# Kernel optimization log

Hardware: AMD Instinct MI355X
Metric: run time of the kernel (lower is better)

## Reference

```python
import jax, jax.numpy as jnp
import numpy as np

EPS = 1e-6


def _build_cayley():
    # Blade ordering of the CEGNN CliffordAlgebra for Cl(3,0): combinations order
    # 1, e1, e2, e3, e12, e13, e23, e123. Metric (1,1,1) => e_k^2 = +1.
    blades = [(), (0,), (1,), (2,), (0, 1), (0, 2), (1, 2), (0, 1, 2)]
    index = {b: i for i, b in enumerate(blades)}
    cayley = np.zeros((8, 8, 8), dtype=np.float32)
    for i, a in enumerate(blades):
        for j, b in enumerate(blades):
            arr = list(a) + list(b)
            sign = 1
            # bubble sort, counting transpositions of anticommuting generators
            for p in range(len(arr)):
                for q in range(len(arr) - 1):
                    if arr[q] > arr[q + 1]:
                        arr[q], arr[q + 1] = arr[q + 1], arr[q]
                        sign = -sign
            # contract equal adjacent generators (e_k e_k = +1)
            out = []
            q = 0
            while q < len(arr):
                if q + 1 < len(arr) and arr[q] == arr[q + 1]:
                    q += 2
                else:
                    out.append(arr[q])
                    q += 1
            cayley[i, j, index[tuple(out)]] = sign
    return cayley


_CAYLEY = jnp.asarray(_build_cayley())  # (8, 8, 8)


def _mvlinear(x, W, b):
    # MVLinear(subspaces=False): channel mixing shared across blades,
    # bias embedded into the scalar (grade-0) blade only.
    y = jnp.einsum("bmi,nm->bni", x, W)
    return y.at[:, :, 0].add(b)


def setup_inputs() -> dict:
    key = jax.random.key(0)
    ks = jax.random.split(key, 7)
    B, Cin, Ch, Cout = 16384, 512, 512, 512
    s = 1.0 / np.sqrt(Cin)
    return {
        "vec1": jax.random.normal(ks[0], (B, Cin, 8), dtype=jnp.float32),
        "W_left": jax.random.normal(ks[1], (Ch, Cin), dtype=jnp.float32) * s,
        "b_left": jax.random.normal(ks[2], (Ch,), dtype=jnp.float32) * 0.01,
        "W_right": jax.random.normal(ks[3], (Ch, Cin), dtype=jnp.float32) * s,
        "b_right": jax.random.normal(ks[4], (Ch,), dtype=jnp.float32) * 0.01,
        "W_out": jax.random.normal(ks[5], (Cout, Ch), dtype=jnp.float32) * s,
        "b_out": jax.random.normal(ks[6], (Cout,), dtype=jnp.float32) * 0.01,
        "a_norm": jnp.ones((Cout,), dtype=jnp.float32),
    }


def reference(vec1, W_left, b_left, W_right, b_right, W_out, b_out, a_norm):
    vec_right = _mvlinear(vec1, W_right, b_right)   # (B, Ch, 8)
    vec_left = _mvlinear(vec1, W_left, b_left)      # (B, Ch, 8)
    # geometric product via the sparse Cayley table of Cl(3,0)
    gp = jnp.einsum("bmi,ijk,bmj->bmk", vec_left, _CAYLEY, vec_right)
    out = _mvlinear(gp, W_out, b_out)               # (B, Cout, 8)
    # MVLayerNorm: per-multivector quadratic-form norm (all-positive metric =>
    # sqrt of sum of squared blade coefficients), averaged over channels.
    norm = jnp.sqrt(jnp.sum(out * out, axis=-1, keepdims=True))  # (B, Cout, 1)
    norm = jnp.mean(norm, axis=1, keepdims=True) + EPS           # (B, 1, 1)
    return a_norm[None, :, None] * out / norm
```

## Files before the change

kernel.cpp:

```cpp
#include <hip/hip_runtime.h>
#include <cstdint>
#include <cstddef>

typedef _Float16 f16;
typedef __attribute__((ext_vector_type(8))) _Float16 f16x8;
typedef __attribute__((ext_vector_type(4))) _Float16 f16x4;
typedef __attribute__((ext_vector_type(4))) float f32x4;

#define MFMA_F16(a, b, c) __builtin_amdgcn_mfma_f32_16x16x32_f16((a), (b), (c), 0, 0, 0)

#define GL2LDS(gsrc, ldst)                                                  \
    __builtin_amdgcn_global_load_lds(                                        \
        (const __attribute__((address_space(1))) void*)(gsrc),               \
        (__attribute__((address_space(3))) void*)(ldst), 16, 0, 0)

#define WAITV(n) asm volatile("s_waitcnt vmcnt(" #n ")" ::: "memory")
#define BAR() __builtin_amdgcn_s_barrier()
#define PRIO(n) __builtin_amdgcn_s_setprio(n)

#define SWZ(row) (((row) >> 1) & 3)


__global__ __launch_bounds__(256) void k0(const float* __restrict__ x,
                                          const float* __restrict__ wl,
                                          const float* __restrict__ wr,
                                          const float* __restrict__ wo,
                                          f16* __restrict__ wdst,
                                          f16* __restrict__ xt) {
    const int bid = blockIdx.x;
    if (bid >= 8192) {
        int i = (bid - 8192) * 256 + threadIdx.x;
        wdst[i]          = (f16)wl[i];
        wdst[262144 + i] = (f16)wr[i];
        wdst[524288 + i] = (f16)wo[i];
        return;
    }
    const int b = (bid >> 1) * 4 + (threadIdx.x >> 6);
    const int m = (bid & 1) * 256 + (threadIdx.x & 63) * 4;
    const float* src = x + ((size_t)b * 512 + m) * 8;
    f32x4 v[8];
#pragma unroll
    for (int u = 0; u < 8; ++u) v[u] = *(const f32x4*)(src + u * 4);
#pragma unroll
    for (int i = 0; i < 8; ++i) {
        f16x4 w;
#pragma unroll
        for (int j = 0; j < 4; ++j) w[j] = (f16)v[j * 2 + (i >> 2)][i & 3];
        *(f16x4*)(xt + (size_t)i * 8388608 + (size_t)b * 512 + m) = w;
    }
}

__global__ __launch_bounds__(512, 2) void k1(
    const f16* __restrict__ xt, const f16* __restrict__ wf,
    const float* __restrict__ bl_p, const float* __restrict__ br_p,
    char* gp_out)
{
    __shared__ __align__(16) f16 AsF[3 * 8192];
    __shared__ __align__(16) f16 BsF[3 * 8192];

    const int L = blockIdx.x;
    const int xcd = L & 7, sl = L >> 3;
    const int bt = xcd * 64 + (sl >> 2), ct = sl & 3;
    const int b0 = bt * 32, n0 = ct * 128;

    const int tid = threadIdx.x, lane = tid & 63, wv = tid >> 6;
    const int wb = wv >> 2, wn = wv & 3;
    const int r_lo = lane & 15, s_hi = lane >> 4;

    const int gA0 = tid, gA1 = tid + 512;
    const int ba0 = gA0 >> 7, ra0 = (gA0 >> 2) & 31, ga0 = (gA0 & 3) ^ SWZ(ra0);
    const int ba1 = gA1 >> 7, ra1 = (gA1 >> 2) & 31, ga1 = (gA1 & 3) ^ SWZ(ra1);
    const f16* aS0 = xt + (size_t)ba0 * 8388608 + (size_t)(b0 + ra0) * 512 + ga0 * 8;
    const f16* aS1 = xt + (size_t)ba1 * 8388608 + (size_t)(b0 + ra1) * 512 + ga1 * 8;
    const int wch = tid >> 2, wg = (tid & 3) ^ SWZ(wch);
    const f16* wS0 = wf + (size_t)(n0 + wch) * 512 + wg * 8;
    const f16* wS1 = wS0 + 262144;

    const int ar = wb * 16 + r_lo;
    const int arow = ar * 32 + ((s_hi ^ SWZ(ar)) << 3);
    int bro[4];
#pragma unroll
    for (int t = 0; t < 4; ++t) {
        const int nrow = ((t & 2) ? 128 : 0) + wn * 32 + (t & 1) * 16 + r_lo;
        bro[t] = nrow * 32 + ((s_hi ^ SWZ(nrow)) << 3);
    }

    f32x4 acc[8][4];
    const f32x4 zero = {0.f, 0.f, 0.f, 0.f};
#pragma unroll
    for (int i = 0; i < 8; ++i)
#pragma unroll
        for (int t = 0; t < 4; ++t) acc[i][t] = zero;

    auto stageA = [&](int kt, int buf) {
        GL2LDS(aS0 + kt * 32, AsF + buf * 8192 + wv * 512);
        GL2LDS(aS1 + kt * 32, AsF + buf * 8192 + 4096 + wv * 512);
    };
    auto stageB = [&](int kt, int buf) {
        GL2LDS(wS0 + kt * 32, BsF + buf * 8192 + wv * 512);
        GL2LDS(wS1 + kt * 32, BsF + buf * 8192 + 4096 + wv * 512);
    };

    stageA(0, 0); stageB(0, 0);
    stageA(1, 1); stageB(1, 1);

#pragma unroll
    for (int kt = 0; kt < 16; ++kt) {
        const int buf = kt % 3, nbuf = (kt + 2) % 3;
        const f16* Ab = AsF + buf * 8192;
        const f16* Bb = BsF + buf * 8192;
        if (kt < 14) stageA(kt + 2, nbuf);
        if (kt <= 13)      { WAITV(6); }
        else if (kt == 14) { WAITV(4); }
        else               { WAITV(0); }
        BAR();
        f16x8 bf[4];
#pragma unroll
        for (int t = 0; t < 4; ++t) bf[t] = *(const f16x8*)(Bb + bro[t]);
        {
            f16x8 a0 = *(const f16x8*)(Ab + 0 * 1024 + arow);
            f16x8 a1 = *(const f16x8*)(Ab + 1 * 1024 + arow);
            f16x8 a2 = *(const f16x8*)(Ab + 2 * 1024 + arow);
            f16x8 a3 = *(const f16x8*)(Ab + 3 * 1024 + arow);
            PRIO(1);
#pragma unroll
            for (int t = 0; t < 4; ++t) {
                acc[0][t] = MFMA_F16(a0, bf[t], acc[0][t]);
                acc[1][t] = MFMA_F16(a1, bf[t], acc[1][t]);
                acc[2][t] = MFMA_F16(a2, bf[t], acc[2][t]);
                acc[3][t] = MFMA_F16(a3, bf[t], acc[3][t]);
            }
            PRIO(0);
        }
        BAR();
        if (kt < 14) stageB(kt + 2, nbuf);
        {
            f16x8 a4 = *(const f16x8*)(Ab + 4 * 1024 + arow);
            f16x8 a5 = *(const f16x8*)(Ab + 5 * 1024 + arow);
            f16x8 a6 = *(const f16x8*)(Ab + 6 * 1024 + arow);
            f16x8 a7 = *(const f16x8*)(Ab + 7 * 1024 + arow);
            PRIO(1);
#pragma unroll
            for (int t = 0; t < 4; ++t) {
                acc[4][t] = MFMA_F16(a4, bf[t], acc[4][t]);
                acc[5][t] = MFMA_F16(a5, bf[t], acc[5][t]);
                acc[6][t] = MFMA_F16(a6, bf[t], acc[6][t]);
                acc[7][t] = MFMA_F16(a7, bf[t], acc[7][t]);
            }
            PRIO(0);
        }
        BAR();
    }

#pragma unroll
    for (int t = 0; t < 2; ++t) {
        const int ch = n0 + wn * 32 + t * 16 + r_lo;
        const float blv = bl_p[ch], brv = br_p[ch];
#pragma unroll
        for (int rr = 0; rr < 4; ++rr) {
            const int b_g = b0 + wb * 16 + s_hi * 4 + rr;
            float Lv[8], Rv[8];
#pragma unroll
            for (int i = 0; i < 8; ++i) { Lv[i] = acc[i][t][rr]; Rv[i] = acc[i][2 + t][rr]; }
            Lv[0] += blv; Rv[0] += brv;
            float g[8];
            g[0] = Lv[0]*Rv[0]+Lv[1]*Rv[1]+Lv[2]*Rv[2]+Lv[3]*Rv[3]-Lv[4]*Rv[4]-Lv[5]*Rv[5]-Lv[6]*Rv[6]-Lv[7]*Rv[7];
            g[1] = Lv[0]*Rv[1]+Lv[1]*Rv[0]-Lv[2]*Rv[4]-Lv[3]*Rv[5]+Lv[4]*Rv[2]+Lv[5]*Rv[3]-Lv[6]*Rv[7]-Lv[7]*Rv[6];
            g[2] = Lv[0]*Rv[2]+Lv[1]*Rv[4]+Lv[2]*Rv[0]-Lv[3]*Rv[6]-Lv[4]*Rv[1]+Lv[5]*Rv[7]+Lv[6]*Rv[3]+Lv[7]*Rv[5];
            g[3] = Lv[0]*Rv[3]+Lv[1]*Rv[5]+Lv[2]*Rv[6]+Lv[3]*Rv[0]-Lv[4]*Rv[7]-Lv[5]*Rv[1]-Lv[6]*Rv[2]-Lv[7]*Rv[4];
            g[4] = Lv[0]*Rv[4]+Lv[1]*Rv[2]-Lv[2]*Rv[1]+Lv[3]*Rv[7]+Lv[4]*Rv[0]-Lv[5]*Rv[6]+Lv[6]*Rv[5]+Lv[7]*Rv[3];
            g[5] = Lv[0]*Rv[5]+Lv[1]*Rv[3]-Lv[2]*Rv[7]-Lv[3]*Rv[1]+Lv[4]*Rv[6]+Lv[5]*Rv[0]-Lv[6]*Rv[4]-Lv[7]*Rv[2];
            g[6] = Lv[0]*Rv[6]+Lv[1]*Rv[7]+Lv[2]*Rv[3]-Lv[3]*Rv[2]-Lv[4]*Rv[5]+Lv[5]*Rv[4]+Lv[6]*Rv[0]+Lv[7]*Rv[1];
            g[7] = Lv[0]*Rv[7]+Lv[1]*Rv[6]-Lv[2]*Rv[5]+Lv[3]*Rv[4]+Lv[4]*Rv[3]-Lv[5]*Rv[2]+Lv[6]*Rv[1]+Lv[7]*Rv[0];
            char* dst = gp_out + (size_t)b_g * 16384 + (size_t)ch * 2;
#pragma unroll
            for (int i = 0; i < 8; ++i) *(f16*)(dst + (size_t)i * 1024) = (f16)g[i];
        }
    }
}

__global__ __launch_bounds__(512, 2) void k2(
    const char* gp_in, const f16* __restrict__ wo,
    const float* __restrict__ bo_p, const float* __restrict__ an_p,
    float* outp)
{
    __shared__ __align__(16) f16 AsF[3 * 4096];
    __shared__ __align__(16) f16 BsF[3 * 16384];
    __shared__ float red[16][8];

    const int b0 = blockIdx.x * 16;
    const int tid = threadIdx.x, lane = tid & 63, wv = tid >> 6;
    const int r_lo = lane & 15, s_hi = lane >> 4;

    const int abl = tid >> 6, arw = (tid >> 2) & 15, agp = (tid & 3) ^ SWZ(arw);
    const char* aS = gp_in + (size_t)(b0 + arw) * 16384 + (size_t)abl * 1024 + agp * 16;
    const f16* bS[4];
#pragma unroll
    for (int j = 0; j < 4; ++j) {
        const int n = j * 128 + (tid >> 2);
        bS[j] = wo + (size_t)n * 512 + ((tid & 3) ^ SWZ(n)) * 8;
    }

    const int aoff = r_lo * 32 + ((s_hi ^ SWZ(r_lo)) << 3);
    int bro[4];
#pragma unroll
    for (int t = 0; t < 4; ++t) {
        const int nrow = wv * 64 + t * 16 + r_lo;
        bro[t] = nrow * 32 + ((s_hi ^ SWZ(nrow)) << 3);
    }

    f32x4 acc[8][4];
    const f32x4 zero = {0.f, 0.f, 0.f, 0.f};
#pragma unroll
    for (int i = 0; i < 8; ++i)
#pragma unroll
        for (int t = 0; t < 4; ++t) acc[i][t] = zero;

    auto stageB01 = [&](int kt, int buf) {
        GL2LDS(bS[0] + kt * 32, BsF + buf * 16384 + 0 * 4096 + wv * 512);
        GL2LDS(bS[1] + kt * 32, BsF + buf * 16384 + 1 * 4096 + wv * 512);
    };
    auto stageAB23 = [&](int kt, int buf) {
        GL2LDS(aS + kt * 64, AsF + buf * 4096 + wv * 512);
        GL2LDS(bS[2] + kt * 32, BsF + buf * 16384 + 2 * 4096 + wv * 512);
        GL2LDS(bS[3] + kt * 32, BsF + buf * 16384 + 3 * 4096 + wv * 512);
    };

    stageB01(0, 0); stageAB23(0, 0);
    stageB01(1, 1); stageAB23(1, 1);

#pragma unroll
    for (int kt = 0; kt < 16; ++kt) {
        const int buf = kt % 3, nbuf = (kt + 2) % 3;
        const f16* Ab = AsF + buf * 4096;
        const f16* Bb = BsF + buf * 16384;
        if (kt < 14) stageB01(kt + 2, nbuf);
        if (kt <= 13)      { WAITV(7); }
        else if (kt == 14) { WAITV(5); }
        else               { WAITV(0); }
        BAR();
        f16x8 af[8];
#pragma unroll
        for (int i = 0; i < 8; ++i) af[i] = *(const f16x8*)(Ab + i * 512 + aoff);
        {
            f16x8 b0f = *(const f16x8*)(Bb + bro[0]);
            f16x8 b1f = *(const f16x8*)(Bb + bro[1]);
            PRIO(1);
#pragma unroll
            for (int i = 0; i < 8; ++i) {
                acc[i][0] = MFMA_F16(af[i], b0f, acc[i][0]);
                acc[i][1] = MFMA_F16(af[i], b1f, acc[i][1]);
            }
            PRIO(0);
        }
        BAR();
        if (kt < 14) stageAB23(kt + 2, nbuf);
        {
            f16x8 b2f = *(const f16x8*)(Bb + bro[2]);
            f16x8 b3f = *(const f16x8*)(Bb + bro[3]);
            PRIO(1);
#pragma unroll
            for (int i = 0; i < 8; ++i) {
                acc[i][2] = MFMA_F16(af[i], b2f, acc[i][2]);
                acc[i][3] = MFMA_F16(af[i], b3f, acc[i][3]);
            }
            PRIO(0);
        }
        BAR();
    }

    float bo_t[4], an_t[4];
#pragma unroll
    for (int t = 0; t < 4; ++t) {
        const int c = wv * 64 + t * 16 + r_lo;
        bo_t[t] = bo_p[c]; an_t[t] = an_p[c];
    }

    float partial[4];
#pragma unroll
    for (int rr = 0; rr < 4; ++rr) {
        float sum = 0.f;
#pragma unroll
        for (int t = 0; t < 4; ++t) {
            float o = acc[0][t][rr] + bo_t[t];
            float ss = o * o;
#pragma unroll
            for (int i = 1; i < 8; ++i) ss += acc[i][t][rr] * acc[i][t][rr];
            sum += sqrtf(ss);
        }
        partial[rr] = sum;
    }
#pragma unroll
    for (int off = 1; off < 16; off <<= 1)
#pragma unroll
        for (int rr = 0; rr < 4; ++rr) partial[rr] += __shfl_xor(partial[rr], off);
    if (r_lo == 0)
#pragma unroll
        for (int rr = 0; rr < 4; ++rr) red[s_hi * 4 + rr][wv] = partial[rr];
    __syncthreads();

#pragma unroll
    for (int rr = 0; rr < 4; ++rr) {
        float tot = 0.f;
#pragma unroll
        for (int w = 0; w < 8; ++w) tot += red[s_hi * 4 + rr][w];
        const float inv = 1.0f / (tot * (1.0f / 512.0f) + 1e-6f);
        const int b_g = b0 + s_hi * 4 + rr;
        float* dst = outp + (size_t)b_g * 4096;
#pragma unroll
        for (int t = 0; t < 4; ++t) {
            const float sc = an_t[t] * inv;
            const int c = wv * 64 + t * 16 + r_lo;
            f32x4 v0, v1;
            v0[0] = (acc[0][t][rr] + bo_t[t]) * sc;
            v0[1] = acc[1][t][rr] * sc; v0[2] = acc[2][t][rr] * sc; v0[3] = acc[3][t][rr] * sc;
            v1[0] = acc[4][t][rr] * sc; v1[1] = acc[5][t][rr] * sc;
            v1[2] = acc[6][t][rr] * sc; v1[3] = acc[7][t][rr] * sc;
            *(f32x4*)(dst + (size_t)c * 8) = v0;
            *(f32x4*)(dst + (size_t)c * 8 + 4) = v1;
        }
    }
}

extern "C" void kernel_launch(void* const* d_in, const int* in_sizes, int n_in,
                              void* d_out, int out_size, void* d_ws, size_t ws_size,
                              hipStream_t stream) {
    const float* x  = (const float*)d_in[0];
    const float* wl = (const float*)d_in[1];
    const float* bl = (const float*)d_in[2];
    const float* wr = (const float*)d_in[3];
    const float* br = (const float*)d_in[4];
    const float* wo = (const float*)d_in[5];
    const float* bo = (const float*)d_in[6];
    const float* an = (const float*)d_in[7];
    f16* wf = (f16*)d_ws;
    f16* xt = wf + (1 << 20);

    hipLaunchKernelGGL(k0, dim3(9216), dim3(256), 0, stream, x, wl, wr, wo, wf, xt);
    hipLaunchKernelGGL(k1, dim3(2048), dim3(512), 0, stream, xt, wf, bl, br, (char*)d_out);
    hipLaunchKernelGGL(k2, dim3(1024), dim3(512), 0, stream,
                       (const char*)d_out, wf + 524288, bo, an, (float*)d_out);
}
```

Before: 408.1 us.

## Load k1 weight fragments directly to registers and halve channel tile

k1 no longer stages the weight tiles through LDS. Each lane now loads its B fragments straight from global memory into double-buffered registers, and the channel tile shrinks from 128 to 64 with twice as many blocks. This removes the B shared-memory buffers and one barrier per k-step, and fewer accumulators allow four blocks per CU. The trade-off is that each A tile in LDS is reused across half as many channels, so activation traffic from L2 doubles, and the per-lane global weight loads may add latency.

After: 489.0 us. 1.2x slower.

```diff
diff --git a/kernel.cpp b/kernel.cpp
--- a/kernel.cpp
+++ b/kernel.cpp
@@ -50,18 +50,17 @@
     }
 }
 
-__global__ __launch_bounds__(512, 2) void k1(
+__global__ __launch_bounds__(512, 4) void k1(
     const f16* __restrict__ xt, const f16* __restrict__ wf,
     const float* __restrict__ bl_p, const float* __restrict__ br_p,
     char* gp_out)
 {
     __shared__ __align__(16) f16 AsF[3 * 8192];
-    __shared__ __align__(16) f16 BsF[3 * 8192];
 
     const int L = blockIdx.x;
     const int xcd = L & 7, sl = L >> 3;
-    const int bt = xcd * 64 + (sl >> 2), ct = sl & 3;
-    const int b0 = bt * 32, n0 = ct * 128;
+    const int bt = xcd * 64 + (sl >> 3), ct = sl & 7;
+    const int b0 = bt * 32, n0 = ct * 64;
 
     const int tid = threadIdx.x, lane = tid & 63, wv = tid >> 6;
     const int wb = wv >> 2, wn = wv & 3;
@@ -72,110 +71,91 @@
     const int ba1 = gA1 >> 7, ra1 = (gA1 >> 2) & 31, ga1 = (gA1 & 3) ^ SWZ(ra1);
     const f16* aS0 = xt + (size_t)ba0 * 8388608 + (size_t)(b0 + ra0) * 512 + ga0 * 8;
     const f16* aS1 = xt + (size_t)ba1 * 8388608 + (size_t)(b0 + ra1) * 512 + ga1 * 8;
-    const int wch = tid >> 2, wg = (tid & 3) ^ SWZ(wch);
-    const f16* wS0 = wf + (size_t)(n0 + wch) * 512 + wg * 8;
-    const f16* wS1 = wS0 + 262144;
 
     const int ar = wb * 16 + r_lo;
     const int arow = ar * 32 + ((s_hi ^ SWZ(ar)) << 3);
-    int bro[4];
-#pragma unroll
-    for (int t = 0; t < 4; ++t) {
-        const int nrow = ((t & 2) ? 128 : 0) + wn * 32 + (t & 1) * 16 + r_lo;
-        bro[t] = nrow * 32 + ((s_hi ^ SWZ(nrow)) << 3);
-    }
-
-    f32x4 acc[8][4];
+
+    const int chrow = n0 + wn * 16 + r_lo;
+    const f16* bPL = wf + (size_t)chrow * 512 + s_hi * 8;
+    const f16* bPR = bPL + 262144;
+
+    f32x4 acc[8][2];
     const f32x4 zero = {0.f, 0.f, 0.f, 0.f};
 #pragma unroll
-    for (int i = 0; i < 8; ++i)
-#pragma unroll
-        for (int t = 0; t < 4; ++t) acc[i][t] = zero;
+    for (int i = 0; i < 8; ++i) { acc[i][0] = zero; acc[i][1] = zero; }
 
     auto stageA = [&](int kt, int buf) {
         GL2LDS(aS0 + kt * 32, AsF + buf * 8192 + wv * 512);
         GL2LDS(aS1 + kt * 32, AsF + buf * 8192 + 4096 + wv * 512);
     };
-    auto stageB = [&](int kt, int buf) {
-        GL2LDS(wS0 + kt * 32, BsF + buf * 8192 + wv * 512);
-        GL2LDS(wS1 + kt * 32, BsF + buf * 8192 + 4096 + wv * 512);
-    };
-
-    stageA(0, 0); stageB(0, 0);
-    stageA(1, 1); stageB(1, 1);
+
+    f16x8 bregs[2][2];
+    bregs[0][0] = *(const f16x8*)bPL;
+    bregs[0][1] = *(const f16x8*)bPR;
+    stageA(0, 0);
+    stageA(1, 1);
 
 #pragma unroll
     for (int kt = 0; kt < 16; ++kt) {
-        const int buf = kt % 3, nbuf = (kt + 2) % 3;
-        const f16* Ab = AsF + buf * 8192;
-        const f16* Bb = BsF + buf * 8192;
-        if (kt < 14) stageA(kt + 2, nbuf);
+        if (kt < 15) {
+            bregs[(kt + 1) & 1][0] = *(const f16x8*)(bPL + (kt + 1) * 32);
+            bregs[(kt + 1) & 1][1] = *(const f16x8*)(bPR + (kt + 1) * 32);
+        }
+        if (kt + 2 < 16) stageA(kt + 2, (kt + 2) % 3);
         if (kt <= 13)      { WAITV(6); }
         else if (kt == 14) { WAITV(4); }
         else               { WAITV(0); }
         BAR();
-        f16x8 bf[4];
-#pragma unroll
-        for (int t = 0; t < 4; ++t) bf[t] = *(const f16x8*)(Bb + bro[t]);
+        const f16* Ab = AsF + (kt % 3) * 8192;
+        const f16x8 bL = bregs[kt & 1][0];
+        const f16x8 bR = bregs[kt & 1][1];
         {
             f16x8 a0 = *(const f16x8*)(Ab + 0 * 1024 + arow);
             f16x8 a1 = *(const f16x8*)(Ab + 1 * 1024 + arow);
             f16x8 a2 = *(const f16x8*)(Ab + 2 * 1024 + arow);
             f16x8 a3 = *(const f16x8*)(Ab + 3 * 1024 + arow);
             PRIO(1);
-#pragma unroll
-            for (int t = 0; t < 4; ++t) {
-                acc[0][t] = MFMA_F16(a0, bf[t], acc[0][t]);
-                acc[1][t] = MFMA_F16(a1, bf[t], acc[1][t]);
-                acc[2][t] = MFMA_F16(a2, bf[t], acc[2][t]);
-                acc[3][t] = MFMA_F16(a3, bf[t], acc[3][t]);
-            }
+            acc[0][0] = MFMA_F16(a0, bL, acc[0][0]); acc[0][1] = MFMA_F16(a0, bR, acc[0][1]);
+            acc[1][0] = MFMA_F16(a1, bL, acc[1][0]); acc[1][1] = MFMA_F16(a1, bR, acc[1][1]);
+            acc[2][0] = MFMA_F16(a2, bL, acc[2][0]); acc[2][1] = MFMA_F16(a2, bR, acc[2][1]);
+            acc[3][0] = MFMA_F16(a3, bL, acc[3][0]); acc[3][1] = MFMA_F16(a3, bR, acc[3][1]);
             PRIO(0);
         }
-        BAR();
-        if (kt < 14) stageB(kt + 2, nbuf);
         {
             f16x8 a4 = *(const f16x8*)(Ab + 4 * 1024 + arow);
             f16x8 a5 = *(const f16x8*)(Ab + 5 * 1024 + arow);
             f16x8 a6 = *(const f16x8*)(Ab + 6 * 1024 + arow);
             f16x8 a7 = *(const f16x8*)(Ab + 7 * 1024 + arow);
             PRIO(1);
-#pragma unroll
-            for (int t = 0; t < 4; ++t) {
-                acc[4][t] = MFMA_F16(a4, bf[t], acc[4][t]);
-                acc[5][t] = MFMA_F16(a5, bf[t], acc[5][t]);
-                acc[6][t] = MFMA_F16(a6, bf[t], acc[6][t]);
-                acc[7][t] = MFMA_F16(a7, bf[t], acc[7][t]);
-            }
+            acc[4][0] = MFMA_F16(a4, bL, acc[4][0]); acc[4][1] = MFMA_F16(a4, bR, acc[4][1]);
+            acc[5][0] = MFMA_F16(a5, bL, acc[5][0]); acc[5][1] = MFMA_F16(a5, bR, acc[5][1]);
+            acc[6][0] = MFMA_F16(a6, bL, acc[6][0]); acc[6][1] = MFMA_F16(a6, bR, acc[6][1]);
+            acc[7][0] = MFMA_F16(a7, bL, acc[7][0]); acc[7][1] = MFMA_F16(a7, bR, acc[7][1]);
             PRIO(0);
         }
         BAR();
     }
 
-#pragma unroll
-    for (int t = 0; t < 2; ++t) {
-        const int ch = n0 + wn * 32 + t * 16 + r_lo;
-        const float blv = bl_p[ch], brv = br_p[ch];
-#pragma unroll
-        for (int rr = 0; rr < 4; ++rr) {
-            const int b_g = b0 + wb * 16 + s_hi * 4 + rr;
-            float Lv[8], Rv[8];
-#pragma unroll
-            for (int i = 0; i < 8; ++i) { Lv[i] = acc[i][t][rr]; Rv[i] = acc[i][2 + t][rr]; }
-            Lv[0] += blv; Rv[0] += brv;
-            float g[8];
-            g[0] = Lv[0]*Rv[0]+Lv[1]*Rv[1]+Lv[2]*Rv[2]+Lv[3]*Rv[3]-Lv[4]*Rv[4]-Lv[5]*Rv[5]-Lv[6]*Rv[6]-Lv[7]*Rv[7];
-            g[1] = Lv[0]*Rv[1]+Lv[1]*Rv[0]-Lv[2]*Rv[4]-Lv[3]*Rv[5]+Lv[4]*Rv[2]+Lv[5]*Rv[3]-Lv[6]*Rv[7]-Lv[7]*Rv[6];
-            g[2] = Lv[0]*Rv[2]+Lv[1]*Rv[4]+Lv[2]*Rv[0]-Lv[3]*Rv[6]-Lv[4]*Rv[1]+Lv[5]*Rv[7]+Lv[6]*Rv[3]+Lv[7]*Rv[5];
-            g[3] = Lv[0]*Rv[3]+Lv[1]*Rv[5]+Lv[2]*Rv[6]+Lv[3]*Rv[0]-Lv[4]*Rv[7]-Lv[5]*Rv[1]-Lv[6]*Rv[2]-Lv[7]*Rv[4];
-            g[4] = Lv[0]*Rv[4]+Lv[1]*Rv[2]-Lv[2]*Rv[1]+Lv[3]*Rv[7]+Lv[4]*Rv[0]-Lv[5]*Rv[6]+Lv[6]*Rv[5]+Lv[7]*Rv[3];
-            g[5] = Lv[0]*Rv[5]+Lv[1]*Rv[3]-Lv[2]*Rv[7]-Lv[3]*Rv[1]+Lv[4]*Rv[6]+Lv[5]*Rv[0]-Lv[6]*Rv[4]-Lv[7]*Rv[2];
-            g[6] = Lv[0]*Rv[6]+Lv[1]*Rv[7]+Lv[2]*Rv[3]-Lv[3]*Rv[2]-Lv[4]*Rv[5]+Lv[5]*Rv[4]+Lv[6]*Rv[0]+Lv[7]*Rv[1];
-            g[7] = Lv[0]*Rv[7]+Lv[1]*Rv[6]-Lv[2]*Rv[5]+Lv[3]*Rv[4]+Lv[4]*Rv[3]-Lv[5]*Rv[2]+Lv[6]*Rv[1]+Lv[7]*Rv[0];
-            char* dst = gp_out + (size_t)b_g * 16384 + (size_t)ch * 2;
-#pragma unroll
-            for (int i = 0; i < 8; ++i) *(f16*)(dst + (size_t)i * 1024) = (f16)g[i];
-        }
+    const float blv = bl_p[chrow], brv = br_p[chrow];
+#pragma unroll
+    for (int rr = 0; rr < 4; ++rr) {
+        const int b_g = b0 + wb * 16 + s_hi * 4 + rr;
+        float Lv[8], Rv[8];
+#pragma unroll
+        for (int i = 0; i < 8; ++i) { Lv[i] = acc[i][0][rr]; Rv[i] = acc[i][1][rr]; }
+        Lv[0] += blv; Rv[0] += brv;
+        float g[8];
+        g[0] = Lv[0]*Rv[0]+Lv[1]*Rv[1]+Lv[2]*Rv[2]+Lv[3]*Rv[3]-Lv[4]*Rv[4]-Lv[5]*Rv[5]-Lv[6]*Rv[6]-Lv[7]*Rv[7];
+        g[1] = Lv[0]*Rv[1]+Lv[1]*Rv[0]-Lv[2]*Rv[4]-Lv[3]*Rv[5]+Lv[4]*Rv[2]+Lv[5]*Rv[3]-Lv[6]*Rv[7]-Lv[7]*Rv[6];
+        g[2] = Lv[0]*Rv[2]+Lv[1]*Rv[4]+Lv[2]*Rv[0]-Lv[3]*Rv[6]-Lv[4]*Rv[1]+Lv[5]*Rv[7]+Lv[6]*Rv[3]+Lv[7]*Rv[5];
+        g[3] = Lv[0]*Rv[3]+Lv[1]*Rv[5]+Lv[2]*Rv[6]+Lv[3]*Rv[0]-Lv[4]*Rv[7]-Lv[5]*Rv[1]-Lv[6]*Rv[2]-Lv[7]*Rv[4];
+        g[4] = Lv[0]*Rv[4]+Lv[1]*Rv[2]-Lv[2]*Rv[1]+Lv[3]*Rv[7]+Lv[4]*Rv[0]-Lv[5]*Rv[6]+Lv[6]*Rv[5]+Lv[7]*Rv[3];
+        g[5] = Lv[0]*Rv[5]+Lv[1]*Rv[3]-Lv[2]*Rv[7]-Lv[3]*Rv[1]+Lv[4]*Rv[6]+Lv[5]*Rv[0]-Lv[6]*Rv[4]-Lv[7]*Rv[2];
+        g[6] = Lv[0]*Rv[6]+Lv[1]*Rv[7]+Lv[2]*Rv[3]-Lv[3]*Rv[2]-Lv[4]*Rv[5]+Lv[5]*Rv[4]+Lv[6]*Rv[0]+Lv[7]*Rv[1];
+        g[7] = Lv[0]*Rv[7]+Lv[1]*Rv[6]-Lv[2]*Rv[5]+Lv[3]*Rv[4]+Lv[4]*Rv[3]-Lv[5]*Rv[2]+Lv[6]*Rv[1]+Lv[7]*Rv[0];
+        char* dst = gp_out + (size_t)b_g * 16384 + (size_t)chrow * 2;
+#pragma unroll
+        for (int i = 0; i < 8; ++i) *(f16*)(dst + (size_t)i * 1024) = (f16)g[i];
     }
 }
 
@@ -337,7 +317,7 @@
     f16* xt = wf + (1 << 20);
 
     hipLaunchKernelGGL(k0, dim3(9216), dim3(256), 0, stream, x, wl, wr, wo, wf, xt);
-    hipLaunchKernelGGL(k1, dim3(2048), dim3(512), 0, stream, xt, wf, bl, br, (char*)d_out);
+    hipLaunchKernelGGL(k1, dim3(4096), dim3(512), 0, stream, xt, wf, bl, br, (char*)d_out);
     hipLaunchKernelGGL(k2, dim3(1024), dim3(512), 0, stream,
                        (const char*)d_out, wf + 524288, bo, an, (float*)d_out);
 }
```

## Double K-tile depth to 64 with double-buffered LDS and scheduling fences

Applied to the files above, without the earlier changes.

The GEMM main loop now stages 64-wide K slices into two LDS buffers, instead of 32-wide slices into three buffers. That halves the loop trip count and the number of barriers and vmcnt waits per unit of K. Each half of the iteration now loads all eight A fragments and issues 32 MFMAs back to back. sched_barrier fences keep the compiler from moving work across the synchronisation points. The trade-off is a larger LDS footprint and a shallower prefetch pipeline (one stage ahead instead of two), which could expose more global-load latency.

New measurement: 410.5 us. About the same (+0.6%).

```diff
diff --git a/kernel.cpp b/kernel.cpp
--- a/kernel.cpp
+++ b/kernel.cpp
@@ -16,6 +16,7 @@
 
 #define WAITV(n) asm volatile("s_waitcnt vmcnt(" #n ")" ::: "memory")
 #define BAR() __builtin_amdgcn_s_barrier()
+#define SCHEDFENCE() __builtin_amdgcn_sched_barrier(0)
 #define PRIO(n) __builtin_amdgcn_s_setprio(n)
 
 #define SWZ(row) (((row) >> 1) & 3)
@@ -55,8 +56,8 @@
     const float* __restrict__ bl_p, const float* __restrict__ br_p,
     char* gp_out)
 {
-    __shared__ __align__(16) f16 AsF[3 * 8192];
-    __shared__ __align__(16) f16 BsF[3 * 8192];
+    __shared__ __align__(16) f16 AsF[2 * 16384];
+    __shared__ __align__(16) f16 BsF[2 * 16384];
 
     const int L = blockIdx.x;
     const int xcd = L & 7, sl = L >> 3;
@@ -93,35 +94,41 @@
         for (int t = 0; t < 4; ++t) acc[i][t] = zero;
 
     auto stageA = [&](int kt, int buf) {
-        GL2LDS(aS0 + kt * 32, AsF + buf * 8192 + wv * 512);
-        GL2LDS(aS1 + kt * 32, AsF + buf * 8192 + 4096 + wv * 512);
+        GL2LDS(aS0 + kt * 64,      AsF + buf * 16384 + wv * 512);
+        GL2LDS(aS1 + kt * 64,      AsF + buf * 16384 + 4096 + wv * 512);
+        GL2LDS(aS0 + kt * 64 + 32, AsF + buf * 16384 + 8192 + wv * 512);
+        GL2LDS(aS1 + kt * 64 + 32, AsF + buf * 16384 + 8192 + 4096 + wv * 512);
     };
     auto stageB = [&](int kt, int buf) {
-        GL2LDS(wS0 + kt * 32, BsF + buf * 8192 + wv * 512);
-        GL2LDS(wS1 + kt * 32, BsF + buf * 8192 + 4096 + wv * 512);
+        GL2LDS(wS0 + kt * 64,      BsF + buf * 16384 + wv * 512);
+        GL2LDS(wS1 + kt * 64,      BsF + buf * 16384 + 4096 + wv * 512);
+        GL2LDS(wS0 + kt * 64 + 32, BsF + buf * 16384 + 8192 + wv * 512);
+        GL2LDS(wS1 + kt * 64 + 32, BsF + buf * 16384 + 8192 + 4096 + wv * 512);
     };
 
     stageA(0, 0); stageB(0, 0);
-    stageA(1, 1); stageB(1, 1);
-
-#pragma unroll
-    for (int kt = 0; kt < 16; ++kt) {
-        const int buf = kt % 3, nbuf = (kt + 2) % 3;
-        const f16* Ab = AsF + buf * 8192;
-        const f16* Bb = BsF + buf * 8192;
-        if (kt < 14) stageA(kt + 2, nbuf);
-        if (kt <= 13)      { WAITV(6); }
-        else if (kt == 14) { WAITV(4); }
-        else               { WAITV(0); }
-        BAR();
-        f16x8 bf[4];
-#pragma unroll
-        for (int t = 0; t < 4; ++t) bf[t] = *(const f16x8*)(Bb + bro[t]);
+
+#pragma unroll
+    for (int kt = 0; kt < 8; ++kt) {
+        const int buf = kt & 1;
+        const f16* Ab = AsF + buf * 16384;
+        const f16* Bb = BsF + buf * 16384;
+        if (kt < 7) stageA(kt + 1, buf ^ 1);
+        if (kt < 7) { WAITV(4); } else { WAITV(0); }
+        BAR();
+        SCHEDFENCE();
         {
+            f16x8 bf[4];
+#pragma unroll
+            for (int t = 0; t < 4; ++t) bf[t] = *(const f16x8*)(Bb + bro[t]);
             f16x8 a0 = *(const f16x8*)(Ab + 0 * 1024 + arow);
             f16x8 a1 = *(const f16x8*)(Ab + 1 * 1024 + arow);
             f16x8 a2 = *(const f16x8*)(Ab + 2 * 1024 + arow);
             f16x8 a3 = *(const f16x8*)(Ab + 3 * 1024 + arow);
+            f16x8 a4 = *(const f16x8*)(Ab + 4 * 1024 + arow);
+            f16x8 a5 = *(const f16x8*)(Ab + 5 * 1024 + arow);
+            f16x8 a6 = *(const f16x8*)(Ab + 6 * 1024 + arow);
+            f16x8 a7 = *(const f16x8*)(Ab + 7 * 1024 + arow);
             PRIO(1);
 #pragma unroll
             for (int t = 0; t < 4; ++t) {
@@ -129,19 +136,6 @@
                 acc[1][t] = MFMA_F16(a1, bf[t], acc[1][t]);
                 acc[2][t] = MFMA_F16(a2, bf[t], acc[2][t]);
                 acc[3][t] = MFMA_F16(a3, bf[t], acc[3][t]);
-            }
-            PRIO(0);
-        }
-        BAR();
-        if (kt < 14) stageB(kt + 2, nbuf);
-        {
-            f16x8 a4 = *(const f16x8*)(Ab + 4 * 1024 + arow);
-            f16x8 a5 = *(const f16x8*)(Ab + 5 * 1024 + arow);
-            f16x8 a6 = *(const f16x8*)(Ab + 6 * 1024 + arow);
-            f16x8 a7 = *(const f16x8*)(Ab + 7 * 1024 + arow);
-            PRIO(1);
-#pragma unroll
-            for (int t = 0; t < 4; ++t) {
                 acc[4][t] = MFMA_F16(a4, bf[t], acc[4][t]);
                 acc[5][t] = MFMA_F16(a5, bf[t], acc[5][t]);
                 acc[6][t] = MFMA_F16(a6, bf[t], acc[6][t]);
@@ -150,6 +144,38 @@
             PRIO(0);
         }
         BAR();
+        SCHEDFENCE();
+        if (kt < 7) stageB(kt + 1, buf ^ 1);
+        {
+            const f16* Ab1 = Ab + 8192;
+            const f16* Bb1 = Bb + 8192;
+            f16x8 bf[4];
+#pragma unroll
+            for (int t = 0; t < 4; ++t) bf[t] = *(const f16x8*)(Bb1 + bro[t]);
+            f16x8 a0 = *(const f16x8*)(Ab1 + 0 * 1024 + arow);
+            f16x8 a1 = *(const f16x8*)(Ab1 + 1 * 1024 + arow);
+            f16x8 a2 = *(const f16x8*)(Ab1 + 2 * 1024 + arow);
+            f16x8 a3 = *(const f16x8*)(Ab1 + 3 * 1024 + arow);
+            f16x8 a4 = *(const f16x8*)(Ab1 + 4 * 1024 + arow);
+            f16x8 a5 = *(const f16x8*)(Ab1 + 5 * 1024 + arow);
+            f16x8 a6 = *(const f16x8*)(Ab1 + 6 * 1024 + arow);
+            f16x8 a7 = *(const f16x8*)(Ab1 + 7 * 1024 + arow);
+            PRIO(1);
+#pragma unroll
+            for (int t = 0; t < 4; ++t) {
+                acc[0][t] = MFMA_F16(a0, bf[t], acc[0][t]);
+                acc[1][t] = MFMA_F16(a1, bf[t], acc[1][t]);
+                acc[2][t] = MFMA_F16(a2, bf[t], acc[2][t]);
+                acc[3][t] = MFMA_F16(a3, bf[t], acc[3][t]);
+                acc[4][t] = MFMA_F16(a4, bf[t], acc[4][t]);
+                acc[5][t] = MFMA_F16(a5, bf[t], acc[5][t]);
+                acc[6][t] = MFMA_F16(a6, bf[t], acc[6][t]);
+                acc[7][t] = MFMA_F16(a7, bf[t], acc[7][t]);
+            }
+            PRIO(0);
+        }
+        BAR();
+        SCHEDFENCE();
     }
 
 #pragma unroll
```

## Rewrite k2 with 1024-thread blocks, register-staged double buffering, fewer accumulators

Applied to the files above, without the earlier changes.

The output GEMM+norm kernel k2 now uses 1024-thread blocks (16 waves), with each wave owning 32 output channels instead of 64, which halves the accumulators per thread. The triple-buffered global_load_lds async pipeline with split barriers is replaced by a simple double buffer staged through registers with one __syncthreads per k-step. The aim is higher occupancy and lower register pressure, at the cost of losing the async direct-to-LDS copies and the finer overlap between loads and MFMA work.

Result: slower. 430.9 us (+5.6%).

```diff
diff --git a/kernel.cpp b/kernel.cpp
--- a/kernel.cpp
+++ b/kernel.cpp
@@ -5,6 +5,7 @@
 typedef _Float16 f16;
 typedef __attribute__((ext_vector_type(8))) _Float16 f16x8;
 typedef __attribute__((ext_vector_type(4))) _Float16 f16x4;
+typedef __attribute__((ext_vector_type(2))) _Float16 f16x2;
 typedef __attribute__((ext_vector_type(4))) float f32x4;
 
 #define MFMA_F16(a, b, c) __builtin_amdgcn_mfma_f32_16x16x32_f16((a), (b), (c), 0, 0, 0)
@@ -179,146 +180,126 @@
     }
 }
 
-__global__ __launch_bounds__(512, 2) void k2(
+__global__ __launch_bounds__(1024, 4) void k2(
     const char* gp_in, const f16* __restrict__ wo,
     const float* __restrict__ bo_p, const float* __restrict__ an_p,
     float* outp)
 {
-    __shared__ __align__(16) f16 AsF[3 * 4096];
-    __shared__ __align__(16) f16 BsF[3 * 16384];
-    __shared__ float red[16][8];
-
-    const int b0 = blockIdx.x * 16;
-    const int tid = threadIdx.x, lane = tid & 63, wv = tid >> 6;
+    __shared__ __align__(16) f16 As[2][8][16*32];
+    __shared__ __align__(16) f16 Bs[2][512*32];
+    __shared__ float red[16][16];
+
+    const int b0   = blockIdx.x * 16;
+    const int tid  = threadIdx.x;
+    const int lane = tid & 63;
+    const int wv   = tid >> 6;
     const int r_lo = lane & 15, s_hi = lane >> 4;
 
-    const int abl = tid >> 6, arw = (tid >> 2) & 15, agp = (tid & 3) ^ SWZ(arw);
-    const char* aS = gp_in + (size_t)(b0 + arw) * 16384 + (size_t)abl * 1024 + agp * 16;
-    const f16* bS[4];
-#pragma unroll
-    for (int j = 0; j < 4; ++j) {
-        const int n = j * 128 + (tid >> 2);
-        bS[j] = wo + (size_t)n * 512 + ((tid & 3) ^ SWZ(n)) * 8;
-    }
-
-    const int aoff = r_lo * 32 + ((s_hi ^ SWZ(r_lo)) << 3);
-    int bro[4];
-#pragma unroll
-    for (int t = 0; t < 4; ++t) {
-        const int nrow = wv * 64 + t * 16 + r_lo;
-        bro[t] = nrow * 32 + ((s_hi ^ SWZ(nrow)) << 3);
-    }
-
-    f32x4 acc[8][4];
+    f32x4 acc[2][8];
     const f32x4 zero = {0.f, 0.f, 0.f, 0.f};
 #pragma unroll
-    for (int i = 0; i < 8; ++i)
-#pragma unroll
-        for (int t = 0; t < 4; ++t) acc[i][t] = zero;
-
-    auto stageB01 = [&](int kt, int buf) {
-        GL2LDS(bS[0] + kt * 32, BsF + buf * 16384 + 0 * 4096 + wv * 512);
-        GL2LDS(bS[1] + kt * 32, BsF + buf * 16384 + 1 * 4096 + wv * 512);
+    for (int st = 0; st < 2; ++st)
+#pragma unroll
+        for (int i = 0; i < 8; ++i) acc[st][i] = zero;
+
+    const int ablade = tid >> 6, arow = (tid >> 2) & 15, ac = tid & 3;
+    const char* asrc0 = gp_in + (size_t)(b0 + arow) * 16384 + (size_t)(ablade & 7) * 1024 + ac * 16;
+    const int aw = arow * 32 + ((ac ^ (arow & 3)) << 3);
+    const int brow = tid >> 1, bc2 = (tid & 1) * 2;
+    const f16* bsrc0 = wo + (size_t)brow * 512 + bc2 * 8;
+    const int bw0 = brow * 32 + (((bc2    ) ^ (brow & 3)) << 3);
+    const int bw1 = brow * 32 + (((bc2 + 1) ^ (brow & 3)) << 3);
+
+    auto stage = [&](int kk, int buf) {
+        if (tid < 512) {
+            f16x8 v = *(const f16x8*)(asrc0 + (size_t)kk * 64);
+            *(f16x8*)&As[buf][ablade][aw] = v;
+        }
+        const f16* bs = bsrc0 + kk * 32;
+        f16x8 v0 = *(const f16x8*)(bs);
+        f16x8 v1 = *(const f16x8*)(bs + 8);
+        *(f16x8*)&Bs[buf][bw0] = v0;
+        *(f16x8*)&Bs[buf][bw1] = v1;
     };
-    auto stageAB23 = [&](int kt, int buf) {
-        GL2LDS(aS + kt * 64, AsF + buf * 4096 + wv * 512);
-        GL2LDS(bS[2] + kt * 32, BsF + buf * 16384 + 2 * 4096 + wv * 512);
-        GL2LDS(bS[3] + kt * 32, BsF + buf * 16384 + 3 * 4096 + wv * 512);
-    };
-
-    stageB01(0, 0); stageAB23(0, 0);
-    stageB01(1, 1); stageAB23(1, 1);
-
-#pragma unroll
-    for (int kt = 0; kt < 16; ++kt) {
-        const int buf = kt % 3, nbuf = (kt + 2) % 3;
-        const f16* Ab = AsF + buf * 4096;
-        const f16* Bb = BsF + buf * 16384;
-        if (kt < 14) stageB01(kt + 2, nbuf);
-        if (kt <= 13)      { WAITV(7); }
-        else if (kt == 14) { WAITV(5); }
-        else               { WAITV(0); }
-        BAR();
-        f16x8 af[8];
-#pragma unroll
-        for (int i = 0; i < 8; ++i) af[i] = *(const f16x8*)(Ab + i * 512 + aoff);
-        {
-            f16x8 b0f = *(const f16x8*)(Bb + bro[0]);
-            f16x8 b1f = *(const f16x8*)(Bb + bro[1]);
-            PRIO(1);
-#pragma unroll
-            for (int i = 0; i < 8; ++i) {
-                acc[i][0] = MFMA_F16(af[i], b0f, acc[i][0]);
-                acc[i][1] = MFMA_F16(af[i], b1f, acc[i][1]);
-            }
-            PRIO(0);
-        }
-        BAR();
-        if (kt < 14) stageAB23(kt + 2, nbuf);
-        {
-            f16x8 b2f = *(const f16x8*)(Bb + bro[2]);
-            f16x8 b3f = *(const f16x8*)(Bb + bro[3]);
-            PRIO(1);
-#pragma unroll
-            for (int i = 0; i < 8; ++i) {
-                acc[i][2] = MFMA_F16(af[i], b2f, acc[i][2]);
-                acc[i][3] = MFMA_F16(af[i], b3f, acc[i][3]);
-            }
-            PRIO(0);
-        }
-        BAR();
-    }
-
-    float bo_t[4], an_t[4];
-#pragma unroll
-    for (int t = 0; t < 4; ++t) {
-        const int c = wv * 64 + t * 16 + r_lo;
-        bo_t[t] = bo_p[c]; an_t[t] = an_p[c];
-    }
+
+    const int nl0 = wv * 32 + r_lo, nl1 = nl0 + 16;
+    const int boff0 = nl0 * 32 + ((s_hi ^ (nl0 & 3)) << 3);
+    const int boff1 = nl1 * 32 + ((s_hi ^ (nl1 & 3)) << 3);
+    const int aoff  = r_lo * 32 + ((s_hi ^ (r_lo & 3)) << 3);
+
+    stage(0, 0);
+    for (int kk = 0; kk < 16; ++kk) {
+        __syncthreads();
+        if (kk < 15) stage(kk + 1, (kk + 1) & 1);
+        const int buf = kk & 1;
+        f16x8 bf0 = *(const f16x8*)&Bs[buf][boff0];
+        f16x8 bf1 = *(const f16x8*)&Bs[buf][boff1];
+#pragma unroll
+        for (int i = 0; i < 8; ++i) {
+            f16x8 a = *(const f16x8*)&As[buf][i][aoff];
+            acc[0][i] = MFMA_F16(a, bf0, acc[0][i]);
+            acc[1][i] = MFMA_F16(a, bf1, acc[1][i]);
+        }
+    }
+
+    const float bo0 = bo_p[nl0], bo1 = bo_p[nl1];
+    const float an0 = an_p[nl0], an1 = an_p[nl1];
 
     float partial[4];
 #pragma unroll
     for (int rr = 0; rr < 4; ++rr) {
-        float sum = 0.f;
-#pragma unroll
-        for (int t = 0; t < 4; ++t) {
-            float o = acc[0][t][rr] + bo_t[t];
-            float ss = o * o;
-#pragma unroll
-            for (int i = 1; i < 8; ++i) ss += acc[i][t][rr] * acc[i][t][rr];
-            sum += sqrtf(ss);
-        }
-        partial[rr] = sum;
-    }
-#pragma unroll
-    for (int off = 1; off < 16; off <<= 1)
+        float o = acc[0][0][rr] + bo0;
+        float ss = o * o;
+#pragma unroll
+        for (int i = 1; i < 8; ++i) ss += acc[0][i][rr] * acc[0][i][rr];
+        float s = sqrtf(ss);
+        o = acc[1][0][rr] + bo1;
+        ss = o * o;
+#pragma unroll
+        for (int i = 1; i < 8; ++i) ss += acc[1][i][rr] * acc[1][i][rr];
+        partial[rr] = s + sqrtf(ss);
+    }
+#pragma unroll
+    for (int off = 1; off < 16; off <<= 1) {
 #pragma unroll
         for (int rr = 0; rr < 4; ++rr) partial[rr] += __shfl_xor(partial[rr], off);
-    if (r_lo == 0)
+    }
+    if (r_lo == 0) {
 #pragma unroll
         for (int rr = 0; rr < 4; ++rr) red[s_hi * 4 + rr][wv] = partial[rr];
+    }
     __syncthreads();
 
 #pragma unroll
     for (int rr = 0; rr < 4; ++rr) {
         float tot = 0.f;
 #pragma unroll
-        for (int w = 0; w < 8; ++w) tot += red[s_hi * 4 + rr][w];
+        for (int w = 0; w < 16; ++w) tot += red[s_hi * 4 + rr][w];
         const float inv = 1.0f / (tot * (1.0f / 512.0f) + 1e-6f);
+        const float sc0 = an0 * inv, sc1 = an1 * inv;
         const int b_g = b0 + s_hi * 4 + rr;
         float* dst = outp + (size_t)b_g * 4096;
-#pragma unroll
-        for (int t = 0; t < 4; ++t) {
-            const float sc = an_t[t] * inv;
-            const int c = wv * 64 + t * 16 + r_lo;
-            f32x4 v0, v1;
-            v0[0] = (acc[0][t][rr] + bo_t[t]) * sc;
-            v0[1] = acc[1][t][rr] * sc; v0[2] = acc[2][t][rr] * sc; v0[3] = acc[3][t][rr] * sc;
-            v1[0] = acc[4][t][rr] * sc; v1[1] = acc[5][t][rr] * sc;
-            v1[2] = acc[6][t][rr] * sc; v1[3] = acc[7][t][rr] * sc;
-            *(f32x4*)(dst + (size_t)c * 8) = v0;
-            *(f32x4*)(dst + (size_t)c * 8 + 4) = v1;
-        }
+        f32x4 v;
+        v[0] = (acc[0][0][rr] + bo0) * sc0;
+        v[1] = acc[0][1][rr] * sc0;
+        v[2] = acc[0][2][rr] * sc0;
+        v[3] = acc[0][3][rr] * sc0;
+        *(f32x4*)(dst + (size_t)nl0 * 8) = v;
+        v[0] = acc[0][4][rr] * sc0;
+        v[1] = acc[0][5][rr] * sc0;
+        v[2] = acc[0][6][rr] * sc0;
+        v[3] = acc[0][7][rr] * sc0;
+        *(f32x4*)(dst + (size_t)nl0 * 8 + 4) = v;
+        v[0] = (acc[1][0][rr] + bo1) * sc1;
+        v[1] = acc[1][1][rr] * sc1;
+        v[2] = acc[1][2][rr] * sc1;
+        v[3] = acc[1][3][rr] * sc1;
+        *(f32x4*)(dst + (size_t)nl1 * 8) = v;
+        v[0] = acc[1][4][rr] * sc1;
+        v[1] = acc[1][5][rr] * sc1;
+        v[2] = acc[1][6][rr] * sc1;
+        v[3] = acc[1][7][rr] * sc1;
+        *(f32x4*)(dst + (size_t)nl1 * 8 + 4) = v;
     }
 }
 
@@ -338,6 +319,6 @@
 
     hipLaunchKernelGGL(k0, dim3(9216), dim3(256), 0, stream, x, wl, wr, wo, wf, xt);
     hipLaunchKernelGGL(k1, dim3(2048), dim3(512), 0, stream, xt, wf, bl, br, (char*)d_out);
-    hipLaunchKernelGGL(k2, dim3(1024), dim3(512), 0, stream,
+    hipLaunchKernelGGL(k2, dim3(1024), dim3(1024), 0, stream,
                        (const char*)d_out, wf + 524288, bo, an, (float*)d_out);
 }
```
